# Kernel tuning notes

Hardware: AMD Instinct MI355X
Metric: run time of the kernel (lower is better)

Reference implementation:

```python
import jax, jax.numpy as jnp
import numpy as np

B, S, H, D = 1, 4096, 16, 64   # batch, seq_len, heads, dim_head (hidden = H*D = 1024)
Q_CHUNK = 512                  # query chunk size; divides S


def setup_inputs() -> dict:
    key = jax.random.key(0)
    kq, kk, kv = jax.random.split(key, 3)
    shape = (B, S, H * D)
    return {
        "query": jax.random.normal(kq, shape, jnp.float32),
        "key": jax.random.normal(kk, shape, jnp.float32),
        "value": jax.random.normal(kv, shape, jnp.float32),
    }


def _heads_to_batch(x):
    # (b, s, h*d) -> (b*h, s, d), matching reshape_heads_to_batch_dim
    b, s, _ = x.shape
    return x.reshape(b, s, H, D).transpose(0, 2, 1, 3).reshape(b * H, s, D)


def _batch_to_heads(x, b):
    # (b*h, s, d) -> (b, s, h*d), matching reshape_batch_dim_to_heads
    bh, s, d = x.shape
    return x.reshape(b, H, s, d).transpose(0, 2, 1, 3).reshape(b, s, H * d)


def reference(query, key, value):
    """Memory-efficient attention path of AttentionOp.apply_attention_dot.

    Math: out = softmax(q k^T / sqrt(dim_head)) v per (batch*head).
    (The mem-efficient path scales by 1/sqrt(k_features); self.scale is unused there.)
    Computed in query chunks to avoid materializing the full [BH, S, S] scores,
    honoring the chunked structure of the original.
    """
    b = query.shape[0]
    q = _heads_to_batch(query) * (1.0 / jnp.sqrt(jnp.float32(D)))  # (BH, S, D)
    k = _heads_to_batch(key)
    v = _heads_to_batch(value)

    n_chunks = q.shape[1] // Q_CHUNK
    # (n_chunks, BH, Q_CHUNK, D)
    qc = q.reshape(-1, n_chunks, Q_CHUNK, D).transpose(1, 0, 2, 3)

    def attend_chunk(qi):
        scores = jnp.einsum("bqd,bkd->bqk", qi, k)        # (BH, C, S)
        probs = jax.nn.softmax(scores, axis=-1)           # stable online-softmax equiv.
        return jnp.einsum("bqk,bkd->bqd", probs, v)       # (BH, C, D)

    oc = jax.lax.map(attend_chunk, qc)                    # (n_chunks, BH, C, D)
    out = oc.transpose(1, 0, 2, 3).reshape(-1, n_chunks * Q_CHUNK, D)
    return _batch_to_heads(out, b)
```

## Files before the change

### kernel.cpp

```cpp
#include <hip/hip_runtime.h>
#include <stdint.h>

typedef __bf16 bf16;
typedef __bf16 bf16x8 __attribute__((ext_vector_type(8)));
typedef float  f32x16 __attribute__((ext_vector_type(16)));

#define S_LEN 4096
#define NHEAD 16
#define HID   1024
#define NTILE 64
#define TILEB 8192
#define QSCALE (0.125f * 1.44269504088896340736f)
#define EXP2F(x) __builtin_amdgcn_exp2f(x)

__device__ __forceinline__ uint32_t pack_bf16(float a, float b) {
    union { bf16 h[2]; uint32_t u; } x;
    x.h[0] = (bf16)a; x.h[1] = (bf16)b;
    return x.u;
}

__global__ __launch_bounds__(256)
void prepack_kernel(const float* __restrict__ Kg, const float* __restrict__ Vg,
                    char* __restrict__ Kb, char* __restrict__ Vb)
{
    const int tile = blockIdx.x, h = blockIdx.y;
    const int t = threadIdx.x;
    __shared__ float Vs[64][65];

    const int key = t >> 2, dq = (t & 3) * 16;
    const float* kp = Kg + (size_t)(tile * 64 + key) * HID + h * 64 + dq;
    const float* vp = Vg + (size_t)(tile * 64 + key) * HID + h * 64 + dq;
    float kv[16], vv[16];
    #pragma unroll
    for (int i = 0; i < 4; ++i) {
        *(float4*)(kv + 4 * i) = *(const float4*)(kp + 4 * i);
        *(float4*)(vv + 4 * i) = *(const float4*)(vp + 4 * i);
    }
    {
        char* kout = Kb + (size_t)(h * NTILE + tile) * TILEB;
        const int i = (t & 3) * 2 + (key >> 5);
        bf16x8 b0, b1;
        #pragma unroll
        for (int e = 0; e < 8; ++e) { b0[e] = (bf16)kv[e]; b1[e] = (bf16)kv[8 + e]; }
        *(bf16x8*)(kout + i * 1024 + (key & 31) * 16)        = b0;
        *(bf16x8*)(kout + i * 1024 + (32 + (key & 31)) * 16) = b1;
    }
    #pragma unroll
    for (int e = 0; e < 16; ++e) Vs[key][dq + e] = vv[e];
    __syncthreads();
    {
        const int d = t >> 2, kq = (t & 3) * 16;
        float tv[16];
        #pragma unroll
        for (int e = 0; e < 16; ++e) tv[e] = Vs[kq + e][d];
        char* vout = Vb + (size_t)(h * NTILE + tile) * TILEB;
        const int j = (t & 3) * 2 + (d >> 5);
        bf16x8 b0, b1;
        #pragma unroll
        for (int e = 0; e < 8; ++e) { b0[e] = (bf16)tv[e]; b1[e] = (bf16)tv[8 + e]; }
        *(bf16x8*)(vout + j * 1024 + (d & 31) * 16)        = b0;
        *(bf16x8*)(vout + j * 1024 + (32 + (d & 31)) * 16) = b1;
    }
}

__global__ __launch_bounds__(256, 4)
void fattn_kernel(const float* __restrict__ Qg,
                  const char* __restrict__ Kb,
                  const char* __restrict__ Vb,
                  float* __restrict__ Og)
{
    const int sb = (blockIdx.x & 7) * 256 + (blockIdx.x >> 3);
    const int h  = sb >> 7;
    const int qc = sb & 127;
    const int t  = threadIdx.x;
    const int w  = t >> 6;
    const int l  = t & 63;
    const int lq = l & 31;
    const int hi = l >> 5;

    __shared__ __attribute__((aligned(16))) float part[3 * 64 * 33];
    char* const obuf = (char*)part;

    bf16x8 qf[4];
    {
        const float* qp = Qg + (size_t)(qc * 32 + lq) * HID + h * 64 + hi * 8;
        #pragma unroll
        for (int kc = 0; kc < 4; ++kc) {
            float tmp[8];
            *(float4*)(tmp)     = *(const float4*)(qp + kc * 16);
            *(float4*)(tmp + 4) = *(const float4*)(qp + kc * 16 + 4);
            #pragma unroll
            for (int e = 0; e < 8; ++e) qf[kc][e] = (bf16)(tmp[e] * QSCALE);
        }
    }

    f32x16 ot0, ot1;
    #pragma unroll
    for (int i = 0; i < 16; ++i) { ot0[i] = 0.f; ot1[i] = 0.f; }
    float lrun = 0.f;

    const char* Khead = Kb + (size_t)h * (NTILE * TILEB) + (size_t)w * 16 * TILEB;
    const char* Vhead = Vb + (size_t)h * (NTILE * TILEB) + (size_t)w * 16 * TILEB;

    for (int it = 0; it < 16; ++it) {
        const char* kt = Khead + (size_t)it * TILEB;
        const char* vt = Vhead + (size_t)it * TILEB;

        #pragma unroll
        for (int khalf = 0; khalf < 2; ++khalf) {
            bf16x8 kfh[4];
            #pragma unroll
            for (int kc = 0; kc < 4; ++kc)
                kfh[kc] = *(const bf16x8*)(kt + (kc * 2 + khalf) * 1024 + l * 16);

            f32x16 sc;
            #pragma unroll
            for (int i = 0; i < 16; ++i) sc[i] = 0.f;
            __builtin_amdgcn_s_setprio(1);
            #pragma unroll
            for (int kc = 0; kc < 4; ++kc)
                sc = __builtin_amdgcn_mfma_f32_32x32x16_bf16(kfh[kc], qf[kc], sc, 0, 0, 0);
            __builtin_amdgcn_s_setprio(0);

            bf16x8 vfh[4];
            #pragma unroll
            for (int j = 0; j < 4; ++j)
                vfh[j] = *(const bf16x8*)(vt + (khalf * 4 + j) * 1024 + l * 16);

            {
                float pa = 0.f, pb = 0.f, pc = 0.f, pd = 0.f;
                #pragma unroll
                for (int i = 0; i < 16; i += 4) {
                    float p0 = EXP2F(sc[i]),     p1 = EXP2F(sc[i + 1]);
                    float p2 = EXP2F(sc[i + 2]), p3 = EXP2F(sc[i + 3]);
                    sc[i] = p0; sc[i + 1] = p1; sc[i + 2] = p2; sc[i + 3] = p3;
                    pa += p0; pb += p1; pc += p2; pd += p3;
                }
                lrun += (pa + pb) + (pc + pd);
            }

            auto pvchunk = [&](int eb, const bf16x8& v0, const bf16x8& v1) {
                uint32_t p0 = pack_bf16(sc[eb + 0], sc[eb + 1]);
                uint32_t p1 = pack_bf16(sc[eb + 2], sc[eb + 3]);
                uint32_t p2 = pack_bf16(sc[eb + 4], sc[eb + 5]);
                uint32_t p3 = pack_bf16(sc[eb + 6], sc[eb + 7]);
                asm volatile("v_permlane32_swap_b32 %0, %1" : "+v"(p0), "+v"(p2));
                asm volatile("v_permlane32_swap_b32 %0, %1" : "+v"(p1), "+v"(p3));
                union { uint32_t w4[4]; bf16x8 v; } pb;
                pb.w4[0] = p0; pb.w4[1] = p1; pb.w4[2] = p2; pb.w4[3] = p3;
                __builtin_amdgcn_s_setprio(1);
                ot0 = __builtin_amdgcn_mfma_f32_32x32x16_bf16(v0, pb.v, ot0, 0, 0, 0);
                ot1 = __builtin_amdgcn_mfma_f32_32x32x16_bf16(v1, pb.v, ot1, 0, 0, 0);
                __builtin_amdgcn_s_setprio(0);
            };
            pvchunk(0, vfh[0], vfh[1]);
            pvchunk(8, vfh[2], vfh[3]);
        }
    }

    lrun += __shfl_xor(lrun, 32);

    if (w > 0) {
        float* pp = part + ((w - 1) * 64 + l) * 33;
        #pragma unroll
        for (int r = 0; r < 16; ++r) { pp[r] = ot0[r]; pp[16 + r] = ot1[r]; }
        pp[32] = lrun;
    }
    __syncthreads();
    if (w == 0) {
        #pragma unroll
        for (int j = 0; j < 3; ++j) {
            const float* pp = part + (j * 64 + l) * 33;
            #pragma unroll
            for (int r = 0; r < 16; ++r) { ot0[r] += pp[r]; ot1[r] += pp[16 + r]; }
            lrun += pp[32];
        }
    }
    __syncthreads();
    if (w == 0) {
        const float inv = 1.f / lrun;
        const int x = (lq & 7) << 4;
        #pragma unroll
        for (int r = 0; r < 16; ++r) {
            const int d0 = (r & 3) + 8 * (r >> 2) + 4 * hi;
            *(float*)(obuf + ((lq * 256 + d0 * 4) ^ x))        = ot0[r] * inv;
            *(float*)(obuf + ((lq * 256 + (32 + d0) * 4) ^ x)) = ot1[r] * inv;
        }
    }
    __syncthreads();
    {
        const int row = t >> 3, oct = t & 7;
        const int x = (row & 7) << 4;
        float* op = Og + (size_t)(qc * 32 + row) * HID + h * 64 + oct * 8;
        float4 v0 = *(const float4*)(obuf + ((row * 256 + oct * 32) ^ x));
        float4 v1 = *(const float4*)(obuf + ((row * 256 + oct * 32 + 16) ^ x));
        *(float4*)(op)     = v0;
        *(float4*)(op + 4) = v1;
    }
}

extern "C" void kernel_launch(void* const* d_in, const int* in_sizes, int n_in,
                              void* d_out, int out_size, void* d_ws, size_t ws_size,
                              hipStream_t stream) {
    const float* Q = (const float*)d_in[0];
    const float* K = (const float*)d_in[1];
    const float* V = (const float*)d_in[2];
    float* O = (float*)d_out;
    char* Kb = (char*)d_ws;
    char* Vb = (char*)d_ws + (size_t)NHEAD * NTILE * TILEB;
    dim3 pgrid(NTILE, NHEAD);
    prepack_kernel<<<pgrid, 256, 0, stream>>>(K, V, Kb, Vb);
    fattn_kernel<<<2048, 256, 0, stream>>>(Q, Kb, Vb, O);
}
```

Measured before the change: 111.3 us.

## Software-pipeline QK^T of next key chunk with softmax and PV of current

Restructures the inner attention loop into a two-stage software pipeline: the QK^T MFMA for the next 32-key chunk is issued while softmax exp and PV MFMAs run on the current chunk, using double-buffered score and K/V register fragments. Occupancy hint is lowered from 4 to 3 waves per SIMD to give room for the extra registers. The goal is to hide MFMA and load latency behind the exp/VALU work. In exchange, register pressure and lower occupancy may reduce latency hiding across waves.

```diff
diff --git a/kernel.cpp b/kernel.cpp
--- a/kernel.cpp
+++ b/kernel.cpp
@@ -63,7 +63,7 @@
     }
 }
 
-__global__ __launch_bounds__(256, 4)
+__global__ __launch_bounds__(256, 3)
 void fattn_kernel(const float* __restrict__ Qg,
                   const char* __restrict__ Kb,
                   const char* __restrict__ Vb,
@@ -102,59 +102,75 @@
     const char* Khead = Kb + (size_t)h * (NTILE * TILEB) + (size_t)w * 16 * TILEB;
     const char* Vhead = Vb + (size_t)h * (NTILE * TILEB) + (size_t)w * 16 * TILEB;
 
-    for (int it = 0; it < 16; ++it) {
-        const char* kt = Khead + (size_t)it * TILEB;
-        const char* vt = Vhead + (size_t)it * TILEB;
-
-        #pragma unroll
-        for (int khalf = 0; khalf < 2; ++khalf) {
-            bf16x8 kfh[4];
-            #pragma unroll
-            for (int kc = 0; kc < 4; ++kc)
-                kfh[kc] = *(const bf16x8*)(kt + (kc * 2 + khalf) * 1024 + l * 16);
-
-            f32x16 sc;
-            #pragma unroll
-            for (int i = 0; i < 16; ++i) sc[i] = 0.f;
-            __builtin_amdgcn_s_setprio(1);
-            #pragma unroll
-            for (int kc = 0; kc < 4; ++kc)
-                sc = __builtin_amdgcn_mfma_f32_32x32x16_bf16(kfh[kc], qf[kc], sc, 0, 0, 0);
-            __builtin_amdgcn_s_setprio(0);
-
-            bf16x8 vfh[4];
-            #pragma unroll
-            for (int j = 0; j < 4; ++j)
-                vfh[j] = *(const bf16x8*)(vt + (khalf * 4 + j) * 1024 + l * 16);
-
-            {
-                float pa = 0.f, pb = 0.f, pc = 0.f, pd = 0.f;
-                #pragma unroll
-                for (int i = 0; i < 16; i += 4) {
-                    float p0 = EXP2F(sc[i]),     p1 = EXP2F(sc[i + 1]);
-                    float p2 = EXP2F(sc[i + 2]), p3 = EXP2F(sc[i + 3]);
-                    sc[i] = p0; sc[i + 1] = p1; sc[i + 2] = p2; sc[i + 3] = p3;
-                    pa += p0; pb += p1; pc += p2; pd += p3;
-                }
-                lrun += (pa + pb) + (pc + pd);
-            }
-
-            auto pvchunk = [&](int eb, const bf16x8& v0, const bf16x8& v1) {
-                uint32_t p0 = pack_bf16(sc[eb + 0], sc[eb + 1]);
-                uint32_t p1 = pack_bf16(sc[eb + 2], sc[eb + 3]);
-                uint32_t p2 = pack_bf16(sc[eb + 4], sc[eb + 5]);
-                uint32_t p3 = pack_bf16(sc[eb + 6], sc[eb + 7]);
-                asm volatile("v_permlane32_swap_b32 %0, %1" : "+v"(p0), "+v"(p2));
-                asm volatile("v_permlane32_swap_b32 %0, %1" : "+v"(p1), "+v"(p3));
-                union { uint32_t w4[4]; bf16x8 v; } pb;
-                pb.w4[0] = p0; pb.w4[1] = p1; pb.w4[2] = p2; pb.w4[3] = p3;
-                __builtin_amdgcn_s_setprio(1);
-                ot0 = __builtin_amdgcn_mfma_f32_32x32x16_bf16(v0, pb.v, ot0, 0, 0, 0);
-                ot1 = __builtin_amdgcn_mfma_f32_32x32x16_bf16(v1, pb.v, ot1, 0, 0, 0);
-                __builtin_amdgcn_s_setprio(0);
-            };
-            pvchunk(0, vfh[0], vfh[1]);
-            pvchunk(8, vfh[2], vfh[3]);
+    auto kload = [&](bf16x8* d, int c) {
+        const char* kt = Khead + (size_t)(c >> 1) * TILEB + (c & 1) * 1024 + l * 16;
+        #pragma unroll
+        for (int kc = 0; kc < 4; ++kc) d[kc] = *(const bf16x8*)(kt + kc * 2048);
+    };
+    auto vload = [&](bf16x8* d, int c) {
+        const char* vt = Vhead + (size_t)(c >> 1) * TILEB + (c & 1) * 4096 + l * 16;
+        #pragma unroll
+        for (int j = 0; j < 4; ++j) d[j] = *(const bf16x8*)(vt + j * 1024);
+    };
+    auto qkt = [&](f32x16& sc, const bf16x8* kf) {
+        #pragma unroll
+        for (int i = 0; i < 16; ++i) sc[i] = 0.f;
+        __builtin_amdgcn_s_setprio(1);
+        #pragma unroll
+        for (int kc = 0; kc < 4; ++kc)
+            sc = __builtin_amdgcn_mfma_f32_32x32x16_bf16(kf[kc], qf[kc], sc, 0, 0, 0);
+        __builtin_amdgcn_s_setprio(0);
+    };
+    auto smx = [&](f32x16& sc) {
+        float pa = 0.f, pb = 0.f, pc = 0.f, pd = 0.f;
+        #pragma unroll
+        for (int i = 0; i < 16; i += 4) {
+            float p0 = EXP2F(sc[i]),     p1 = EXP2F(sc[i + 1]);
+            float p2 = EXP2F(sc[i + 2]), p3 = EXP2F(sc[i + 3]);
+            sc[i] = p0; sc[i + 1] = p1; sc[i + 2] = p2; sc[i + 3] = p3;
+            pa += p0; pb += p1; pc += p2; pd += p3;
+        }
+        lrun += (pa + pb) + (pc + pd);
+    };
+    auto pvchunk = [&](const f32x16& sc, int eb, const bf16x8& v0, const bf16x8& v1) {
+        uint32_t p0 = pack_bf16(sc[eb + 0], sc[eb + 1]);
+        uint32_t p1 = pack_bf16(sc[eb + 2], sc[eb + 3]);
+        uint32_t p2 = pack_bf16(sc[eb + 4], sc[eb + 5]);
+        uint32_t p3 = pack_bf16(sc[eb + 6], sc[eb + 7]);
+        asm volatile("v_permlane32_swap_b32 %0, %1" : "+v"(p0), "+v"(p2));
+        asm volatile("v_permlane32_swap_b32 %0, %1" : "+v"(p1), "+v"(p3));
+        union { uint32_t w4[4]; bf16x8 v; } pb;
+        pb.w4[0] = p0; pb.w4[1] = p1; pb.w4[2] = p2; pb.w4[3] = p3;
+        __builtin_amdgcn_s_setprio(1);
+        ot0 = __builtin_amdgcn_mfma_f32_32x32x16_bf16(v0, pb.v, ot0, 0, 0, 0);
+        ot1 = __builtin_amdgcn_mfma_f32_32x32x16_bf16(v1, pb.v, ot1, 0, 0, 0);
+        __builtin_amdgcn_s_setprio(0);
+    };
+    auto pv = [&](const f32x16& sc, const bf16x8* vf) {
+        pvchunk(sc, 0, vf[0], vf[1]);
+        pvchunk(sc, 8, vf[2], vf[3]);
+    };
+
+    f32x16 scA, scB;
+    bf16x8 kA[4], kB[4], vA[4], vB[4];
+    kload(kA, 0);
+    qkt(scA, kA);
+    vload(vA, 0);
+    for (int c = 0; c < 32; c += 2) {
+        kload(kB, c + 1);
+        smx(scA);
+        qkt(scB, kB);
+        vload(vB, c + 1);
+        pv(scA, vA);
+        if (c + 2 < 32) {
+            kload(kA, c + 2);
+            smx(scB);
+            qkt(scA, kA);
+            vload(vA, c + 2);
+            pv(scB, vB);
+        } else {
+            smx(scB);
+            pv(scB, vB);
         }
     }
 
```

After: 143.4 us, median of 3. +28.8%, slower.

## Process 64 queries per block with two-way key split instead of four

Applied to the files above, without the earlier changes.

Each block now covers 64 query rows split across two wave pairs, and each pair divides the key range in two. Previously 32 queries were split across four waves. This halves the grid and the number of times K/V tiles are streamed per head, reducing global/L2 traffic, and simplifies the final cross-wave reduction to a single partial. In exchange each wave runs twice as many key iterations, lengthening per-block latency and reducing parallel slack.

```diff
diff --git a/kernel.cpp b/kernel.cpp
--- a/kernel.cpp
+++ b/kernel.cpp
@@ -69,21 +69,23 @@
                   const char* __restrict__ Vb,
                   float* __restrict__ Og)
 {
-    const int sb = (blockIdx.x & 7) * 256 + (blockIdx.x >> 3);
-    const int h  = sb >> 7;
-    const int qc = sb & 127;
+    const int sb = (blockIdx.x & 7) * 128 + (blockIdx.x >> 3);
+    const int h  = sb >> 6;
+    const int qc = sb & 63;
     const int t  = threadIdx.x;
     const int w  = t >> 6;
+    const int qg = w >> 1;
+    const int ws = w & 1;
     const int l  = t & 63;
     const int lq = l & 31;
     const int hi = l >> 5;
 
-    __shared__ __attribute__((aligned(16))) float part[3 * 64 * 33];
+    __shared__ __attribute__((aligned(16))) float part[2 * 64 * 33];
     char* const obuf = (char*)part;
 
     bf16x8 qf[4];
     {
-        const float* qp = Qg + (size_t)(qc * 32 + lq) * HID + h * 64 + hi * 8;
+        const float* qp = Qg + (size_t)(qc * 64 + qg * 32 + lq) * HID + h * 64 + hi * 8;
         #pragma unroll
         for (int kc = 0; kc < 4; ++kc) {
             float tmp[8];
@@ -99,10 +101,10 @@
     for (int i = 0; i < 16; ++i) { ot0[i] = 0.f; ot1[i] = 0.f; }
     float lrun = 0.f;
 
-    const char* Khead = Kb + (size_t)h * (NTILE * TILEB) + (size_t)w * 16 * TILEB;
-    const char* Vhead = Vb + (size_t)h * (NTILE * TILEB) + (size_t)w * 16 * TILEB;
-
-    for (int it = 0; it < 16; ++it) {
+    const char* Khead = Kb + (size_t)h * (NTILE * TILEB) + (size_t)ws * 32 * TILEB;
+    const char* Vhead = Vb + (size_t)h * (NTILE * TILEB) + (size_t)ws * 32 * TILEB;
+
+    for (int it = 0; it < 32; ++it) {
         const char* kt = Khead + (size_t)it * TILEB;
         const char* vt = Vhead + (size_t)it * TILEB;
 
@@ -160,42 +162,43 @@
 
     lrun += __shfl_xor(lrun, 32);
 
-    if (w > 0) {
-        float* pp = part + ((w - 1) * 64 + l) * 33;
+    if (ws == 1) {
+        float* pp = part + (qg * 64 + l) * 33;
         #pragma unroll
         for (int r = 0; r < 16; ++r) { pp[r] = ot0[r]; pp[16 + r] = ot1[r]; }
         pp[32] = lrun;
     }
     __syncthreads();
-    if (w == 0) {
-        #pragma unroll
-        for (int j = 0; j < 3; ++j) {
-            const float* pp = part + (j * 64 + l) * 33;
-            #pragma unroll
-            for (int r = 0; r < 16; ++r) { ot0[r] += pp[r]; ot1[r] += pp[16 + r]; }
-            lrun += pp[32];
-        }
-    }
-    __syncthreads();
-    if (w == 0) {
+    if (ws == 0) {
+        const float* pp = part + (qg * 64 + l) * 33;
+        #pragma unroll
+        for (int r = 0; r < 16; ++r) { ot0[r] += pp[r]; ot1[r] += pp[16 + r]; }
+        lrun += pp[32];
+    }
+    __syncthreads();
+    if (ws == 0) {
         const float inv = 1.f / lrun;
+        char* ob = obuf + qg * 8192;
         const int x = (lq & 7) << 4;
         #pragma unroll
         for (int r = 0; r < 16; ++r) {
             const int d0 = (r & 3) + 8 * (r >> 2) + 4 * hi;
-            *(float*)(obuf + ((lq * 256 + d0 * 4) ^ x))        = ot0[r] * inv;
-            *(float*)(obuf + ((lq * 256 + (32 + d0) * 4) ^ x)) = ot1[r] * inv;
-        }
-    }
-    __syncthreads();
-    {
-        const int row = t >> 3, oct = t & 7;
-        const int x = (row & 7) << 4;
-        float* op = Og + (size_t)(qc * 32 + row) * HID + h * 64 + oct * 8;
-        float4 v0 = *(const float4*)(obuf + ((row * 256 + oct * 32) ^ x));
-        float4 v1 = *(const float4*)(obuf + ((row * 256 + oct * 32 + 16) ^ x));
-        *(float4*)(op)     = v0;
-        *(float4*)(op + 4) = v1;
+            *(float*)(ob + ((lq * 256 + d0 * 4) ^ x))        = ot0[r] * inv;
+            *(float*)(ob + ((lq * 256 + (32 + d0) * 4) ^ x)) = ot1[r] * inv;
+        }
+    }
+    __syncthreads();
+    {
+        const int row = t >> 2, quarter = t & 3;
+        const int qloc = row & 31;
+        const int x = (qloc & 7) << 4;
+        const char* ob = obuf + (row >> 5) * 8192;
+        float* op = Og + (size_t)(qc * 64 + row) * HID + h * 64 + quarter * 16;
+        #pragma unroll
+        for (int i = 0; i < 4; ++i) {
+            float4 v = *(const float4*)(ob + ((qloc * 256 + quarter * 64 + i * 16) ^ x));
+            *(float4*)(op + i * 4) = v;
+        }
     }
 }
 
@@ -210,5 +213,5 @@
     char* Vb = (char*)d_ws + (size_t)NHEAD * NTILE * TILEB;
     dim3 pgrid(NTILE, NHEAD);
     prepack_kernel<<<pgrid, 256, 0, stream>>>(K, V, Kb, Vb);
-    fattn_kernel<<<2048, 256, 0, stream>>>(Q, Kb, Vb, O);
-}
+    fattn_kernel<<<1024, 256, 0, stream>>>(Q, Kb, Vb, O);
+}
```

Result: faster. 107.2 us, median of 2 (-3.7%).
